# Kernel optimization log

Hardware: AMD Instinct MI355X
Metric: run time of the kernel (lower is better)

Reference implementation:

```python
import jax, jax.numpy as jnp
import numpy as np

D_MODEL = 1024
EXPAND = 2
D_INNER = D_MODEL * EXPAND  # 2048
D_STATE = 16
D_CONV = 4
B, T = 4, 2048


def setup_inputs() -> dict:
    key = jax.random.key(0)
    ks = jax.random.split(key, 8)
    s = 0.02  # small init std for numeric stability
    return {
        "x": jax.random.normal(ks[0], (B, T, D_MODEL), jnp.float32),
        "in_proj_w": jax.random.normal(ks[1], (2 * D_INNER, D_MODEL), jnp.float32) * s,
        "conv_w": jax.random.normal(ks[2], (D_INNER, 1, D_CONV), jnp.float32) * s,
        "conv_b": jnp.zeros((D_INNER,), jnp.float32),
        "x_proj_w": jax.random.normal(ks[3], (2 * D_STATE, D_INNER), jnp.float32) * s,
        "dt_proj_w": jax.random.normal(ks[4], (D_INNER, D_STATE), jnp.float32) * s,
        "dt_proj_b": jnp.zeros((D_INNER,), jnp.float32),
        "D_param": jnp.ones((D_INNER,), jnp.float32),
        "out_proj_w": jax.random.normal(ks[5], (D_MODEL, D_INNER), jnp.float32) * s,
    }


def reference(x, in_proj_w, conv_w, conv_b, x_proj_w, dt_proj_w, dt_proj_b, D_param, out_proj_w):
    Bsz, Tlen, _ = x.shape
    # in_proj (no bias), torch Linear: x @ W.T
    xz = jnp.einsum('btd,ed->bte', x, in_proj_w)            # [B,T,2*D_INNER]
    x_inner, z = jnp.split(xz, 2, axis=-1)                   # each [B,T,D_INNER]
    # depthwise causal conv1d: left-pad d_conv-1, take first T outputs
    xc = jnp.transpose(x_inner, (0, 2, 1))                   # [B,D_INNER,T]
    xc = jax.lax.conv_general_dilated(
        xc, conv_w, window_strides=(1,), padding=[(D_CONV - 1, 0)],
        feature_group_count=D_INNER)
    xc = xc + conv_b[None, :, None]
    x_conv = jax.nn.silu(jnp.transpose(xc, (0, 2, 1)))       # [B,T,D_INNER]
    # x_proj -> (B_ssm, C_ssm); C_ssm is unused by the simplified scan (faithful)
    x_ssm = jnp.einsum('btd,ed->bte', x_conv, x_proj_w)      # [B,T,2*D_STATE]
    B_ssm, C_ssm = jnp.split(x_ssm, 2, axis=-1)
    dt = jax.nn.softplus(jnp.einsum('btn,dn->btd', B_ssm, dt_proj_w) + dt_proj_b)  # [B,T,D_INNER]
    # simplified selective scan: EMA with scalar-per-timestep gate
    alpha = jax.nn.sigmoid(jnp.mean(dt, axis=-1, keepdims=True))  # [B,T,1]

    def step(h, inp):
        a, xt = inp
        h = a * h + (1.0 - a) * xt
        return h, h

    aT = jnp.transpose(alpha, (1, 0, 2))   # [T,B,1]
    xT = jnp.transpose(x_conv, (1, 0, 2))  # [T,B,D_INNER]
    h0 = jnp.zeros((Bsz, D_INNER), x.dtype)
    _, ys = jax.lax.scan(step, h0, (aT, xT))
    y = jnp.transpose(ys, (1, 0, 2))        # [B,T,D_INNER]
    y = y * D_param + x_conv                # skip with learned D
    y = y * jax.nn.silu(z)                  # gate
    out = jnp.einsum('btd,ed->bte', y, out_proj_w)  # [B,T,D_MODEL]
    return out
```

## Files before the change

kernel.cpp:

```cpp
#include <hip/hip_runtime.h>
#include <stdint.h>

#define TLEN   2048
#define DMODEL 1024
#define DINNER 2048
#define MROWS  8192
#define NCH    16
#define CHUNK  128

typedef unsigned short u16;
typedef __bf16 bf16x8 __attribute__((ext_vector_type(8)));
typedef float  f32x4  __attribute__((ext_vector_type(4)));

__device__ __forceinline__ float bf2f(u16 u) {
  union { unsigned int i; float f; } v; v.i = ((unsigned int)u) << 16; return v.f;
}
__device__ __forceinline__ u16 f2bf(float f) {
  union { float f; unsigned int u; } v; v.f = f;
  unsigned int u = v.u;
  return (u16)((u + 0x7fffu + ((u >> 16) & 1u)) >> 16);
}
__device__ __forceinline__ float silu_f(float x) { return x / (1.f + __expf(-x)); }

__device__ __forceinline__ void async16(const u16* g, u16* l) {
  __builtin_amdgcn_global_load_lds(
      (const __attribute__((address_space(1))) void*)(g),
      (__attribute__((address_space(3))) void*)(l),
      16, 0, 0);
}

__global__ __launch_bounds__(256) void k_convert(const float* __restrict__ x,
    const float* __restrict__ w1, const float* __restrict__ w3,
    const float* __restrict__ xpw,
    u16* __restrict__ xb, u16* __restrict__ w1b, u16* __restrict__ w3b,
    u16* __restrict__ xpwb) {
  int i = blockIdx.x * 256 + threadIdx.x;
  const int nx  = MROWS * DMODEL / 4;
  const int nw1 = 2 * DINNER * DMODEL / 4;
  const int nw3 = DMODEL * DINNER / 4;
  const float* src; u16* dst; int j;
  if (i < nx)                  { src = x;   dst = xb;   j = i; }
  else if (i < nx + nw1)       { src = w1;  dst = w1b;  j = i - nx; }
  else if (i < nx + nw1 + nw3) { src = w3;  dst = w3b;  j = i - nx - nw1; }
  else                         { src = xpw; dst = xpwb; j = i - nx - nw1 - nw3; }
  float4 v = ((const float4*)src)[j];
  ushort4 o;
  o.x = f2bf(v.x); o.y = f2bf(v.y); o.z = f2bf(v.z); o.w = f2bf(v.w);
  ((ushort4*)dst)[j] = o;
}

template<int N, int K, bool OUT_BF16>
__global__ __launch_bounds__(256) void k_gemm_bt(const u16* __restrict__ A,
    const u16* __restrict__ B, void* __restrict__ C) {
  __shared__ u16 sA[128 * 32];
  __shared__ u16 sB[128 * 32];
  const int tid  = threadIdx.x;
  const int lane = tid & 63;
  const int wave = tid >> 6;
  const int wm   = (wave >> 1) * 64;
  const int wn   = (wave & 1) * 64;
  const int fr   = lane & 15;
  const int q    = lane >> 4;
  const size_t blockM = (size_t)blockIdx.y * 128;
  const size_t blockN = (size_t)blockIdx.x * 128;

  const int srow = lane >> 2;
  const int scol = (lane & 3) * 8;
  const u16* gA = A + (blockM + (size_t)wave * 32 + srow) * (size_t)K + scol;
  const u16* gB = B + (blockN + (size_t)wave * 32 + srow) * (size_t)K + scol;
  u16* lA = sA + wave * 1024;
  u16* lB = sB + wave * 1024;

  f32x4 acc[4][4] = {};

  for (int kt = 0; kt < K; kt += 32) {
    async16(gA + kt,                   lA);
    async16(gA + 16 * (size_t)K + kt,  lA + 512);
    async16(gB + kt,                   lB);
    async16(gB + 16 * (size_t)K + kt,  lB + 512);
    __syncthreads();

    bf16x8 af[4], bfr[4];
    #pragma unroll
    for (int tm = 0; tm < 4; tm++)
      af[tm] = *(const bf16x8*)(sA + (wm + tm * 16 + fr) * 32 + q * 8);
    #pragma unroll
    for (int tn = 0; tn < 4; tn++)
      bfr[tn] = *(const bf16x8*)(sB + (wn + tn * 16 + fr) * 32 + q * 8);
    #pragma unroll
    for (int tm = 0; tm < 4; tm++)
      #pragma unroll
      for (int tn = 0; tn < 4; tn++)
        acc[tm][tn] = __builtin_amdgcn_mfma_f32_16x16x32_bf16(
            af[tm], bfr[tn], acc[tm][tn], 0, 0, 0);
    __syncthreads();
  }

  #pragma unroll
  for (int tm = 0; tm < 4; tm++)
    #pragma unroll
    for (int tn = 0; tn < 4; tn++)
      #pragma unroll
      for (int r = 0; r < 4; r++) {
        size_t row = blockM + wm + tm * 16 + q * 4 + r;
        size_t col = blockN + wn + tn * 16 + fr;
        float v = acc[tm][tn][r];
        if (OUT_BF16) ((u16*)C)[row * N + col] = f2bf(v);
        else          ((float*)C)[row * N + col] = v;
      }
}

__global__ __launch_bounds__(256) void k_conv(const u16* __restrict__ xz,
    const float* __restrict__ cw, const float* __restrict__ cb,
    u16* __restrict__ xc) {
  int idx = blockIdx.x * 256 + threadIdx.x;
  int d  = idx & (DINNER - 1);
  int tb = (idx >> 11) & 255;
  int b  = idx >> 19;
  float4 w = ((const float4*)cw)[d];
  float bias = cb[d];
  const u16* inp = xz + ((size_t)(b * TLEN + tb * 8)) * 4096 + d;
  float v[11];
  #pragma unroll
  for (int j = 0; j < 11; j++) {
    int t = tb * 8 - 3 + j;
    v[j] = (t >= 0) ? bf2f(inp[(ptrdiff_t)(j - 3) * 4096]) : 0.f;
  }
  u16* outp = xc + ((size_t)(b * TLEN + tb * 8)) * DINNER + d;
  #pragma unroll
  for (int i = 0; i < 8; i++) {
    float acc = bias + w.x * v[i] + w.y * v[i + 1] + w.z * v[i + 2] + w.w * v[i + 3];
    outp[(size_t)i * DINNER] = f2bf(silu_f(acc));
  }
}

__global__ __launch_bounds__(256) void k_bssm(const u16* __restrict__ xc,
    const u16* __restrict__ xpwb, float* __restrict__ bssm) {
  const int tid  = threadIdx.x;
  const int lane = tid & 63;
  const int wave = tid >> 6;
  const int fr   = lane & 15;
  const int q    = lane >> 4;
  const size_t row0 = (size_t)blockIdx.x * 32;
  const int k0 = wave * 512;

  f32x4 acc[2] = {};
  #pragma unroll
  for (int kk = 0; kk < 512; kk += 32) {
    const int kb = k0 + kk + q * 8;
    bf16x8 bfrag = *(const bf16x8*)(xpwb + (size_t)fr * DINNER + kb);
    #pragma unroll
    for (int tm = 0; tm < 2; tm++) {
      bf16x8 afrag = *(const bf16x8*)(xc + (row0 + tm * 16 + fr) * (size_t)DINNER + kb);
      acc[tm] = __builtin_amdgcn_mfma_f32_16x16x32_bf16(afrag, bfrag, acc[tm], 0, 0, 0);
    }
  }

  __shared__ float red[4][32][16];
  #pragma unroll
  for (int tm = 0; tm < 2; tm++)
    #pragma unroll
    for (int r = 0; r < 4; r++)
      red[wave][tm * 16 + q * 4 + r][fr] = acc[tm][r];
  __syncthreads();
  #pragma unroll
  for (int i = tid; i < 512; i += 256) {
    int r = i >> 4, n = i & 15;
    bssm[(row0 + r) * 16 + n] =
        red[0][r][n] + red[1][r][n] + red[2][r][n] + red[3][r][n];
  }
}

__global__ __launch_bounds__(256) void k_alpha(const float* __restrict__ bssm,
    const float* __restrict__ dtw, const float* __restrict__ dtb,
    float* __restrict__ alpha) {
  const int tid = threadIdx.x;
  const size_t row0 = (size_t)blockIdx.x * 16;
  __shared__ float4 sB[16][4];
  { int r = tid >> 4, n = tid & 15;
    ((float*)&sB[r][0])[n] = bssm[(row0 + r) * 16 + n]; }
  __syncthreads();

  float rowsum[16];
  #pragma unroll
  for (int r = 0; r < 16; r++) rowsum[r] = 0.f;

  #pragma unroll 1
  for (int m = 0; m < 4; m++) {
    const int d0 = m * 512 + tid * 2;
    float4 w[2][4]; float bias[2];
    #pragma unroll
    for (int j = 0; j < 2; j++) {
      const float4* wp = (const float4*)(dtw + (size_t)(d0 + j) * 16);
      w[j][0] = wp[0]; w[j][1] = wp[1]; w[j][2] = wp[2]; w[j][3] = wp[3];
      bias[j] = dtb[d0 + j];
    }
    #pragma unroll
    for (int r = 0; r < 16; r++) {
      float4 b0 = sB[r][0], b1 = sB[r][1], b2 = sB[r][2], b3 = sB[r][3];
      float s = 0.f;
      #pragma unroll
      for (int j = 0; j < 2; j++) {
        float dot = bias[j]
          + b0.x * w[j][0].x + b0.y * w[j][0].y + b0.z * w[j][0].z + b0.w * w[j][0].w
          + b1.x * w[j][1].x + b1.y * w[j][1].y + b1.z * w[j][1].z + b1.w * w[j][1].w
          + b2.x * w[j][2].x + b2.y * w[j][2].y + b2.z * w[j][2].z + b2.w * w[j][2].w
          + b3.x * w[j][3].x + b3.y * w[j][3].y + b3.z * w[j][3].z + b3.w * w[j][3].w;
        s += (dot > 15.f) ? dot : __logf(1.f + __expf(dot));
      }
      rowsum[r] += s;
    }
  }
  #pragma unroll
  for (int r = 0; r < 16; r++)
    #pragma unroll
    for (int off = 32; off > 0; off >>= 1) rowsum[r] += __shfl_xor(rowsum[r], off);
  __shared__ float red[4][16];
  if ((tid & 63) == 0) {
    #pragma unroll
    for (int r = 0; r < 16; r++) red[tid >> 6][r] = rowsum[r];
  }
  __syncthreads();
  if (tid < 16) {
    float mean = (red[0][tid] + red[1][tid] + red[2][tid] + red[3][tid]) * (1.f / DINNER);
    alpha[row0 + tid] = 1.f / (1.f + __expf(-mean));
  }
}

__global__ __launch_bounds__(256) void k_scan1(const u16* __restrict__ xc,
    const float* __restrict__ alpha, float* __restrict__ carry) {
  const int blk = blockIdx.x;
  const int g = blk & 7;
  const int c = (blk >> 3) & 15;
  const int b = blk >> 7;
  const int d = g * 256 + threadIdx.x;
  __shared__ float sa[CHUNK];
  if (threadIdx.x < CHUNK) sa[threadIdx.x] = alpha[b * TLEN + c * CHUNK + threadIdx.x];
  __syncthreads();
  const u16* xp = xc + ((size_t)(b * TLEN + c * CHUNK)) * DINNER + d;
  float h = 0.f;
  #pragma unroll 8
  for (int i = 0; i < CHUNK; i++) {
    float a = sa[i];
    float xv = bf2f(xp[(size_t)i * DINNER]);
    h = a * h + (1.f - a) * xv;
  }
  carry[((size_t)(b * NCH + c)) * DINNER + d] = h;
}

__global__ __launch_bounds__(256) void k_scan2(float* __restrict__ carry,
    const float* __restrict__ alpha) {
  int i = blockIdx.x * 256 + threadIdx.x;
  int b = i >> 11;
  int d = i & (DINNER - 1);
  __shared__ float sP[NCH];
  if (threadIdx.x < NCH) {
    const float* ap = alpha + b * TLEN + threadIdx.x * CHUNK;
    float p = 1.f;
    for (int j = 0; j < CHUNK; j++) p *= ap[j];
    sP[threadIdx.x] = p;
  }
  __syncthreads();
  float h = 0.f;
  #pragma unroll
  for (int c = 0; c < NCH; c++) {
    size_t idx = ((size_t)(b * NCH + c)) * DINNER + d;
    float cv = carry[idx];
    carry[idx] = h;
    h = sP[c] * h + cv;
  }
}

__global__ __launch_bounds__(256) void k_scan3(const u16* __restrict__ xc,
    const u16* __restrict__ xz, const float* __restrict__ alpha,
    const float* __restrict__ Hs, const float* __restrict__ Dp,
    u16* __restrict__ yg) {
  const int blk = blockIdx.x;
  const int g = blk & 7;
  const int c = (blk >> 3) & 15;
  const int b = blk >> 7;
  const int d = g * 256 + threadIdx.x;
  __shared__ float sa[CHUNK];
  if (threadIdx.x < CHUNK) sa[threadIdx.x] = alpha[b * TLEN + c * CHUNK + threadIdx.x];
  __syncthreads();
  float h = Hs[((size_t)(b * NCH + c)) * DINNER + d];
  const float Dv = Dp[d];
  const size_t row0 = (size_t)(b * TLEN + c * CHUNK);
  #pragma unroll 4
  for (int i = 0; i < CHUNK; i++) {
    size_t row = row0 + i;
    float a = sa[i];
    float xv = bf2f(xc[row * DINNER + d]);
    h = a * h + (1.f - a) * xv;
    float zv = bf2f(xz[row * 4096 + DINNER + d]);
    float y = h * Dv + xv;
    yg[row * DINNER + d] = f2bf(y * silu_f(zv));
  }
}

extern "C" void kernel_launch(void* const* d_in, const int* in_sizes, int n_in,
                              void* d_out, int out_size, void* d_ws, size_t ws_size,
                              hipStream_t stream) {
  const float* x   = (const float*)d_in[0];
  const float* w1  = (const float*)d_in[1];
  const float* cw  = (const float*)d_in[2];
  const float* cb  = (const float*)d_in[3];
  const float* xpw = (const float*)d_in[4];
  const float* dtw = (const float*)d_in[5];
  const float* dtb = (const float*)d_in[6];
  const float* Dp  = (const float*)d_in[7];
  const float* w3  = (const float*)d_in[8];
  float* out = (float*)d_out;
  char* ws = (char*)d_ws;

  u16*   xb    = (u16*)(ws + 0);
  u16*   w1b   = (u16*)(ws + 16777216);
  u16*   w3b   = (u16*)(ws + 25165824);
  u16*   xz    = (u16*)(ws + 29360128);
  u16*   xc    = (u16*)(ws + 96468992);
  u16*   yg    = (u16*)(ws + 130023424);
  float* bssm  = (float*)(ws + 163577856);
  float* alpha = (float*)(ws + 164102144);
  float* carry = (float*)(ws + 164135168);
  u16*   xpwb  = (u16*)(ws + 164659456);

  k_convert  <<<14368, 256, 0, stream>>>(x, w1, w3, xpw, xb, w1b, w3b, xpwb);
  k_gemm_bt<4096, 1024, true ><<<dim3(32, 64), 256, 0, stream>>>(xb, w1b, xz);
  k_conv     <<<8192, 256, 0, stream>>>(xz, cw, cb, xc);
  k_bssm     <<<256, 256, 0, stream>>>(xc, xpwb, bssm);
  k_alpha    <<<512, 256, 0, stream>>>(bssm, dtw, dtb, alpha);
  k_scan1    <<<512, 256, 0, stream>>>(xc, alpha, carry);
  k_scan2    <<<32, 256, 0, stream>>>(carry, alpha);
  k_scan3    <<<512, 256, 0, stream>>>(xc, xz, alpha, carry, Dp, yg);
  k_gemm_bt<1024, 2048, false><<<dim3(8, 64), 256, 0, stream>>>(yg, w3b, out);
}
```

Measured before the change: 343.0 us.

## Fuse conv, B projection, alpha and chunk carry into one front kernel

Merges the depthwise conv, the B_ssm projection, the alpha computation and the per-16-step chunk scan into a single kernel. The conv output tile stays in shared memory for the MFMA projection and the local scan, so xc is no longer reread from global memory. The separate carry-propagation kernel is removed; each scan block now serially combines up to 120 prefix carries of 16 steps on its own. This saves several launches and passes over xc, but adds a longer serial prefix loop in the scan and large shared-memory use per block, which limits occupancy.

```diff
diff --git a/kernel.cpp b/kernel.cpp
--- a/kernel.cpp
+++ b/kernel.cpp
@@ -5,8 +5,8 @@
 #define DMODEL 1024
 #define DINNER 2048
 #define MROWS  8192
-#define NCH    16
 #define CHUNK  128
+#define FRPAD  2064
 
 typedef unsigned short u16;
 typedef __bf16 bf16x8 __attribute__((ext_vector_type(8)));
@@ -27,6 +27,21 @@
       (const __attribute__((address_space(1))) void*)(g),
       (__attribute__((address_space(3))) void*)(l),
       16, 0, 0);
+}
+
+__device__ __forceinline__ void unpack8(uint4 raw, float* v) {
+  v[0] = bf2f(raw.x & 0xffff); v[1] = bf2f(raw.x >> 16);
+  v[2] = bf2f(raw.y & 0xffff); v[3] = bf2f(raw.y >> 16);
+  v[4] = bf2f(raw.z & 0xffff); v[5] = bf2f(raw.z >> 16);
+  v[6] = bf2f(raw.w & 0xffff); v[7] = bf2f(raw.w >> 16);
+}
+__device__ __forceinline__ uint4 pack8(const u16* o) {
+  uint4 r;
+  r.x = (unsigned)o[0] | ((unsigned)o[1] << 16);
+  r.y = (unsigned)o[2] | ((unsigned)o[3] << 16);
+  r.z = (unsigned)o[4] | ((unsigned)o[5] << 16);
+  r.w = (unsigned)o[6] | ((unsigned)o[7] << 16);
+  return r;
 }
 
 __global__ __launch_bounds__(256) void k_convert(const float* __restrict__ x,
@@ -110,98 +125,102 @@
       }
 }
 
-__global__ __launch_bounds__(256) void k_conv(const u16* __restrict__ xz,
-    const float* __restrict__ cw, const float* __restrict__ cb,
-    u16* __restrict__ xc) {
-  int idx = blockIdx.x * 256 + threadIdx.x;
-  int d  = idx & (DINNER - 1);
-  int tb = (idx >> 11) & 255;
-  int b  = idx >> 19;
-  float4 w = ((const float4*)cw)[d];
-  float bias = cb[d];
-  const u16* inp = xz + ((size_t)(b * TLEN + tb * 8)) * 4096 + d;
-  float v[11];
-  #pragma unroll
-  for (int j = 0; j < 11; j++) {
-    int t = tb * 8 - 3 + j;
-    v[j] = (t >= 0) ? bf2f(inp[(ptrdiff_t)(j - 3) * 4096]) : 0.f;
-  }
-  u16* outp = xc + ((size_t)(b * TLEN + tb * 8)) * DINNER + d;
-  #pragma unroll
-  for (int i = 0; i < 8; i++) {
-    float acc = bias + w.x * v[i] + w.y * v[i + 1] + w.z * v[i + 2] + w.w * v[i + 3];
-    outp[(size_t)i * DINNER] = f2bf(silu_f(acc));
-  }
-}
-
-__global__ __launch_bounds__(256) void k_bssm(const u16* __restrict__ xc,
-    const u16* __restrict__ xpwb, float* __restrict__ bssm) {
-  const int tid  = threadIdx.x;
+__global__ __launch_bounds__(256) void k_front(
+    const u16* __restrict__ xz, const float* __restrict__ cw,
+    const float* __restrict__ cb, const u16* __restrict__ xpwb,
+    const float* __restrict__ dtw, const float* __restrict__ dtb,
+    u16* __restrict__ xc, float* __restrict__ alpha,
+    float* __restrict__ P16, float* __restrict__ carry16) {
+  __shared__ u16   sxc[16 * FRPAD];
+  __shared__ float red[4][16][16];
+  __shared__ float sB[16][16];
+  __shared__ float redA[4][16];
+  __shared__ float salpha[16];
+
+  const int tid = threadIdx.x;
+  const int c16 = blockIdx.x & 127;
+  const int b   = blockIdx.x >> 7;
+  const int t0  = c16 * 16;
+  const size_t row0 = (size_t)b * TLEN + t0;
+  const int d0  = tid * 8;
+
+  float w0[8], w1[8], w2[8], w3[8], bias[8];
+  #pragma unroll
+  for (int j = 0; j < 8; j++) {
+    float4 w = ((const float4*)cw)[d0 + j];
+    w0[j] = w.x; w1[j] = w.y; w2[j] = w.z; w3[j] = w.w;
+    bias[j] = cb[d0 + j];
+  }
+  float p3[8], p2[8], p1[8], cur[8];
+  #pragma unroll
+  for (int j = 0; j < 8; j++) { p3[j] = 0.f; p2[j] = 0.f; p1[j] = 0.f; }
+  if (t0 >= 3) {
+    uint4 r3 = *(const uint4*)(xz + ((size_t)(b * TLEN + t0 - 3)) * 4096 + d0);
+    uint4 r2 = *(const uint4*)(xz + ((size_t)(b * TLEN + t0 - 2)) * 4096 + d0);
+    uint4 r1 = *(const uint4*)(xz + ((size_t)(b * TLEN + t0 - 1)) * 4096 + d0);
+    unpack8(r3, p3); unpack8(r2, p2); unpack8(r1, p1);
+  }
+  #pragma unroll 4
+  for (int r = 0; r < 16; r++) {
+    uint4 rc = *(const uint4*)(xz + (row0 + r) * 4096 + d0);
+    unpack8(rc, cur);
+    u16 o[8];
+    #pragma unroll
+    for (int j = 0; j < 8; j++) {
+      float a = bias[j] + w0[j] * p3[j] + w1[j] * p2[j] + w2[j] * p1[j] + w3[j] * cur[j];
+      o[j] = f2bf(silu_f(a));
+    }
+    uint4 pk = pack8(o);
+    *(uint4*)(xc + (row0 + r) * DINNER + d0) = pk;
+    *(uint4*)(&sxc[r * FRPAD + d0]) = pk;
+    #pragma unroll
+    for (int j = 0; j < 8; j++) { p3[j] = p2[j]; p2[j] = p1[j]; p1[j] = cur[j]; }
+  }
+  __syncthreads();
+
   const int lane = tid & 63;
   const int wave = tid >> 6;
   const int fr   = lane & 15;
   const int q    = lane >> 4;
-  const size_t row0 = (size_t)blockIdx.x * 32;
-  const int k0 = wave * 512;
-
-  f32x4 acc[2] = {};
-  #pragma unroll
-  for (int kk = 0; kk < 512; kk += 32) {
-    const int kb = k0 + kk + q * 8;
-    bf16x8 bfrag = *(const bf16x8*)(xpwb + (size_t)fr * DINNER + kb);
-    #pragma unroll
-    for (int tm = 0; tm < 2; tm++) {
-      bf16x8 afrag = *(const bf16x8*)(xc + (row0 + tm * 16 + fr) * (size_t)DINNER + kb);
-      acc[tm] = __builtin_amdgcn_mfma_f32_16x16x32_bf16(afrag, bfrag, acc[tm], 0, 0, 0);
+  {
+    f32x4 acc = {};
+    const int k0 = wave * 512;
+    #pragma unroll
+    for (int kk = 0; kk < 512; kk += 32) {
+      const int kb = k0 + kk + q * 8;
+      bf16x8 af = *(const bf16x8*)(&sxc[fr * FRPAD + kb]);
+      bf16x8 bf_ = *(const bf16x8*)(xpwb + (size_t)fr * DINNER + kb);
+      acc = __builtin_amdgcn_mfma_f32_16x16x32_bf16(af, bf_, acc, 0, 0, 0);
     }
-  }
-
-  __shared__ float red[4][32][16];
-  #pragma unroll
-  for (int tm = 0; tm < 2; tm++)
-    #pragma unroll
-    for (int r = 0; r < 4; r++)
-      red[wave][tm * 16 + q * 4 + r][fr] = acc[tm][r];
-  __syncthreads();
-  #pragma unroll
-  for (int i = tid; i < 512; i += 256) {
-    int r = i >> 4, n = i & 15;
-    bssm[(row0 + r) * 16 + n] =
-        red[0][r][n] + red[1][r][n] + red[2][r][n] + red[3][r][n];
-  }
-}
-
-__global__ __launch_bounds__(256) void k_alpha(const float* __restrict__ bssm,
-    const float* __restrict__ dtw, const float* __restrict__ dtb,
-    float* __restrict__ alpha) {
-  const int tid = threadIdx.x;
-  const size_t row0 = (size_t)blockIdx.x * 16;
-  __shared__ float4 sB[16][4];
+    #pragma unroll
+    for (int r = 0; r < 4; r++) red[wave][q * 4 + r][fr] = acc[r];
+  }
+  __syncthreads();
   { int r = tid >> 4, n = tid & 15;
-    ((float*)&sB[r][0])[n] = bssm[(row0 + r) * 16 + n]; }
+    sB[r][n] = red[0][r][n] + red[1][r][n] + red[2][r][n] + red[3][r][n]; }
   __syncthreads();
 
   float rowsum[16];
   #pragma unroll
   for (int r = 0; r < 16; r++) rowsum[r] = 0.f;
-
   #pragma unroll 1
   for (int m = 0; m < 4; m++) {
-    const int d0 = m * 512 + tid * 2;
-    float4 w[2][4]; float bias[2];
+    const int dd = m * 512 + tid * 2;
+    float4 w[2][4]; float bs[2];
     #pragma unroll
     for (int j = 0; j < 2; j++) {
-      const float4* wp = (const float4*)(dtw + (size_t)(d0 + j) * 16);
+      const float4* wp = (const float4*)(dtw + (size_t)(dd + j) * 16);
       w[j][0] = wp[0]; w[j][1] = wp[1]; w[j][2] = wp[2]; w[j][3] = wp[3];
-      bias[j] = dtb[d0 + j];
+      bs[j] = dtb[dd + j];
     }
     #pragma unroll
     for (int r = 0; r < 16; r++) {
-      float4 b0 = sB[r][0], b1 = sB[r][1], b2 = sB[r][2], b3 = sB[r][3];
+      const float4* bp = (const float4*)sB[r];
+      float4 b0 = bp[0], b1 = bp[1], b2 = bp[2], b3 = bp[3];
       float s = 0.f;
       #pragma unroll
       for (int j = 0; j < 2; j++) {
-        float dot = bias[j]
+        float dot = bs[j]
           + b0.x * w[j][0].x + b0.y * w[j][0].y + b0.z * w[j][0].z + b0.w * w[j][0].w
           + b1.x * w[j][1].x + b1.y * w[j][1].y + b1.z * w[j][1].z + b1.w * w[j][1].w
           + b2.x * w[j][2].x + b2.y * w[j][2].y + b2.z * w[j][2].z + b2.w * w[j][2].w
@@ -215,20 +234,46 @@
   for (int r = 0; r < 16; r++)
     #pragma unroll
     for (int off = 32; off > 0; off >>= 1) rowsum[r] += __shfl_xor(rowsum[r], off);
-  __shared__ float red[4][16];
   if ((tid & 63) == 0) {
     #pragma unroll
-    for (int r = 0; r < 16; r++) red[tid >> 6][r] = rowsum[r];
+    for (int r = 0; r < 16; r++) redA[tid >> 6][r] = rowsum[r];
   }
   __syncthreads();
   if (tid < 16) {
-    float mean = (red[0][tid] + red[1][tid] + red[2][tid] + red[3][tid]) * (1.f / DINNER);
-    alpha[row0 + tid] = 1.f / (1.f + __expf(-mean));
-  }
-}
-
-__global__ __launch_bounds__(256) void k_scan1(const u16* __restrict__ xc,
-    const float* __restrict__ alpha, float* __restrict__ carry) {
+    float mean = (redA[0][tid] + redA[1][tid] + redA[2][tid] + redA[3][tid]) * (1.f / DINNER);
+    float a = 1.f / (1.f + __expf(-mean));
+    alpha[row0 + tid] = a;
+    salpha[tid] = a;
+  }
+  __syncthreads();
+
+  if (tid == 0) {
+    float p = salpha[0];
+    #pragma unroll
+    for (int r = 1; r < 16; r++) p *= salpha[r];
+    P16[b * 128 + c16] = p;
+  }
+  float h[8];
+  #pragma unroll
+  for (int j = 0; j < 8; j++) h[j] = 0.f;
+  #pragma unroll 4
+  for (int r = 0; r < 16; r++) {
+    float a = salpha[r];
+    float xv[8];
+    unpack8(*(const uint4*)(&sxc[r * FRPAD + d0]), xv);
+    #pragma unroll
+    for (int j = 0; j < 8; j++) h[j] = a * h[j] + (1.f - a) * xv[j];
+  }
+  float4* cp = (float4*)(carry16 + ((size_t)(b * 128 + c16)) * DINNER + d0);
+  float4 h0 = { h[0], h[1], h[2], h[3] };
+  float4 h1 = { h[4], h[5], h[6], h[7] };
+  cp[0] = h0; cp[1] = h1;
+}
+
+__global__ __launch_bounds__(256) void k_scan(const u16* __restrict__ xc,
+    const u16* __restrict__ xz, const float* __restrict__ alpha,
+    const float* __restrict__ P16, const float* __restrict__ carry16,
+    const float* __restrict__ Dp, u16* __restrict__ yg) {
   const int blk = blockIdx.x;
   const int g = blk & 7;
   const int c = (blk >> 3) & 15;
@@ -237,53 +282,15 @@
   __shared__ float sa[CHUNK];
   if (threadIdx.x < CHUNK) sa[threadIdx.x] = alpha[b * TLEN + c * CHUNK + threadIdx.x];
   __syncthreads();
-  const u16* xp = xc + ((size_t)(b * TLEN + c * CHUNK)) * DINNER + d;
+
   float h = 0.f;
-  #pragma unroll 8
-  for (int i = 0; i < CHUNK; i++) {
-    float a = sa[i];
-    float xv = bf2f(xp[(size_t)i * DINNER]);
-    h = a * h + (1.f - a) * xv;
-  }
-  carry[((size_t)(b * NCH + c)) * DINNER + d] = h;
-}
-
-__global__ __launch_bounds__(256) void k_scan2(float* __restrict__ carry,
-    const float* __restrict__ alpha) {
-  int i = blockIdx.x * 256 + threadIdx.x;
-  int b = i >> 11;
-  int d = i & (DINNER - 1);
-  __shared__ float sP[NCH];
-  if (threadIdx.x < NCH) {
-    const float* ap = alpha + b * TLEN + threadIdx.x * CHUNK;
-    float p = 1.f;
-    for (int j = 0; j < CHUNK; j++) p *= ap[j];
-    sP[threadIdx.x] = p;
-  }
-  __syncthreads();
-  float h = 0.f;
-  #pragma unroll
-  for (int c = 0; c < NCH; c++) {
-    size_t idx = ((size_t)(b * NCH + c)) * DINNER + d;
-    float cv = carry[idx];
-    carry[idx] = h;
-    h = sP[c] * h + cv;
-  }
-}
-
-__global__ __launch_bounds__(256) void k_scan3(const u16* __restrict__ xc,
-    const u16* __restrict__ xz, const float* __restrict__ alpha,
-    const float* __restrict__ Hs, const float* __restrict__ Dp,
-    u16* __restrict__ yg) {
-  const int blk = blockIdx.x;
-  const int g = blk & 7;
-  const int c = (blk >> 3) & 15;
-  const int b = blk >> 7;
-  const int d = g * 256 + threadIdx.x;
-  __shared__ float sa[CHUNK];
-  if (threadIdx.x < CHUNK) sa[threadIdx.x] = alpha[b * TLEN + c * CHUNK + threadIdx.x];
-  __syncthreads();
-  float h = Hs[((size_t)(b * NCH + c)) * DINNER + d];
+  const int ccend = c * 8;
+  for (int cc = 0; cc < ccend; cc++) {
+    float p  = P16[b * 128 + cc];
+    float cv = carry16[((size_t)(b * 128 + cc)) * DINNER + d];
+    h = p * h + cv;
+  }
+
   const float Dv = Dp[d];
   const size_t row0 = (size_t)(b * TLEN + c * CHUNK);
   #pragma unroll 4
@@ -313,24 +320,20 @@
   float* out = (float*)d_out;
   char* ws = (char*)d_ws;
 
-  u16*   xb    = (u16*)(ws + 0);
-  u16*   w1b   = (u16*)(ws + 16777216);
-  u16*   w3b   = (u16*)(ws + 25165824);
-  u16*   xz    = (u16*)(ws + 29360128);
-  u16*   xc    = (u16*)(ws + 96468992);
-  u16*   yg    = (u16*)(ws + 130023424);
-  float* bssm  = (float*)(ws + 163577856);
-  float* alpha = (float*)(ws + 164102144);
-  float* carry = (float*)(ws + 164135168);
-  u16*   xpwb  = (u16*)(ws + 164659456);
-
-  k_convert  <<<14368, 256, 0, stream>>>(x, w1, w3, xpw, xb, w1b, w3b, xpwb);
+  u16*   xb      = (u16*)(ws + 0);
+  u16*   w1b     = (u16*)(ws + 16777216);
+  u16*   w3b     = (u16*)(ws + 25165824);
+  u16*   xz      = (u16*)(ws + 29360128);
+  u16*   xc      = (u16*)(ws + 96468992);
+  u16*   yg      = (u16*)(ws + 130023424);
+  u16*   xpwb    = (u16*)(ws + 163577856);
+  float* alpha   = (float*)(ws + 163643392);
+  float* P16     = (float*)(ws + 163676160);
+  float* carry16 = (float*)(ws + 0);
+
+  k_convert<<<14368, 256, 0, stream>>>(x, w1, w3, xpw, xb, w1b, w3b, xpwb);
   k_gemm_bt<4096, 1024, true ><<<dim3(32, 64), 256, 0, stream>>>(xb, w1b, xz);
-  k_conv     <<<8192, 256, 0, stream>>>(xz, cw, cb, xc);
-  k_bssm     <<<256, 256, 0, stream>>>(xc, xpwb, bssm);
-  k_alpha    <<<512, 256, 0, stream>>>(bssm, dtw, dtb, alpha);
-  k_scan1    <<<512, 256, 0, stream>>>(xc, alpha, carry);
-  k_scan2    <<<32, 256, 0, stream>>>(carry, alpha);
-  k_scan3    <<<512, 256, 0, stream>>>(xc, xz, alpha, carry, Dp, yg);
+  k_front  <<<512, 256, 0, stream>>>(xz, cw, cb, xpwb, dtw, dtb, xc, alpha, P16, carry16);
+  k_scan   <<<512, 256, 0, stream>>>(xc, xz, alpha, P16, carry16, Dp, yg);
   k_gemm_bt<1024, 2048, false><<<dim3(8, 64), 256, 0, stream>>>(yg, w3b, out);
 }
```

After: 364.6 us. +6.3%, slower.
